# Performance work log

Hardware: AMD Instinct MI355X
Metric: run time of the kernel (lower is better)

## Reference

```python
import jax, jax.numpy as jnp
import numpy as np

T, TRACE, CTX = 4096, 64, 64


def setup_inputs() -> dict:
    key = jax.random.key(0)
    k0, k1, k2, k3 = jax.random.split(key, 4)
    state_re = jax.random.normal(k0, (T, TRACE, CTX), dtype=jnp.float32)
    state_im = jax.random.normal(k1, (T, TRACE, CTX), dtype=jnp.float32)
    x_re = jax.random.normal(k2, (T, TRACE, CTX), dtype=jnp.float32)
    x_im = jax.random.normal(k3, (T, TRACE, CTX), dtype=jnp.float32)
    # deterministic FFA param init (init_deterministic)
    a = jnp.linspace(1e-6, 0.5, TRACE).astype(jnp.float32)
    b = (2.0 * jnp.pi / jnp.linspace(1.0, 1000.0, CTX)).astype(jnp.float32)
    i = jnp.ones((T,), dtype=jnp.int32)          # carry step counter
    j = jnp.arange(T, dtype=jnp.int32)           # incoming time offsets
    return {"state_re": state_re, "state_im": state_im, "x_re": x_re,
            "x_im": x_im, "a": a, "b": b, "i": i, "j": j}


def reference(state_re, state_im, x_re, x_im, a, b, i, j):
    # gamma(t) = exp((-|a| + i*b) * t) expanded in real arithmetic
    t = j.astype(jnp.float32)[:, None, None]              # [T,1,1]
    decay = jnp.exp(-jnp.abs(a)[None, :, None] * t)       # [T,TRACE,1]
    theta = b[None, None, :] * t                          # [T,1,CTX]
    g_re = decay * jnp.cos(theta)                         # [T,TRACE,CTX]
    g_im = decay * jnp.sin(theta)
    # state * gamma + x  (complex multiply-add)
    new_re = state_re * g_re - state_im * g_im + x_re
    new_im = state_re * g_im + state_im * g_re + x_im
    # output: complex state stacked as (..., 2) = (re, im), plus updated counter
    return jnp.stack([new_re, new_im], axis=-1), j + i
```

## Files before the change

kernel.cpp:

```cpp
#include <hip/hip_runtime.h>
#include <math.h>

#define T_DIM 4096
#define TRACE 64
#define CTX   64
#define NELEM  (T_DIM * TRACE * CTX)
#define NGROUP (NELEM / 4)

typedef float f32x4 __attribute__((ext_vector_type(4)));

__global__ __launch_bounds__(256) void ffm_tables(
    const float* __restrict__ a, const float* __restrict__ b,
    const int*   __restrict__ iv, const int* __restrict__ jv,
    float* __restrict__ tcos, float* __restrict__ tsin,
    float* __restrict__ tdec, float* __restrict__ out_cnt)
{
    const int idx = blockIdx.x * 256 + threadIdx.x;
    const int t   = idx >> 6;
    const int k   = idx & 63;
    const float tf = (float)jv[t];
    float s, c;
    sincosf(b[k] * tf, &s, &c);
    tcos[idx] = c;
    tsin[idx] = s;
    tdec[idx] = expf(-fabsf(a[k]) * tf);
    if (k == 0) out_cnt[t] = (float)(jv[t] + iv[t]);
}

__global__ __launch_bounds__(256) void ffm_main(
    const float* __restrict__ sre_, const float* __restrict__ sim_,
    const float* __restrict__ xre_, const float* __restrict__ xim_,
    const float* __restrict__ tcos, const float* __restrict__ tsin,
    const float* __restrict__ tdec,
    float* __restrict__ out)
{
    const float4* __restrict__ sre = (const float4*)sre_;
    const float4* __restrict__ sim = (const float4*)sim_;
    const float4* __restrict__ xre = (const float4*)xre_;
    const float4* __restrict__ xim = (const float4*)xim_;
    f32x4* __restrict__ o = (f32x4*)out;

    const int stride = gridDim.x * 256;
    const int g0 = blockIdx.x * 256 + threadIdx.x;

    #pragma unroll 2
    for (int it = 0; it < NGROUP / (2048 * 256); ++it) {
        const int g  = g0 + it * stride;
        const int e  = g << 2;
        const int t  = e >> 12;
        const int tr = (e >> 6) & 63;
        const int c0 = e & 63;

        const float4 vc  = *(const float4*)(tcos + t * 64 + c0);
        const float4 vs  = *(const float4*)(tsin + t * 64 + c0);
        const float  dec = tdec[t * 64 + tr];

        const float4 vre = sre[g];
        const float4 vim = sim[g];
        const float4 vxr = xre[g];
        const float4 vxi = xim[g];

        const float gr0 = dec * vc.x, gi0 = dec * vs.x;
        const float gr1 = dec * vc.y, gi1 = dec * vs.y;
        const float gr2 = dec * vc.z, gi2 = dec * vs.z;
        const float gr3 = dec * vc.w, gi3 = dec * vs.w;

        f32x4 o0, o1;
        o0.x = fmaf(vre.x, gr0, fmaf(-vim.x, gi0, vxr.x));
        o0.y = fmaf(vre.x, gi0, fmaf( vim.x, gr0, vxi.x));
        o0.z = fmaf(vre.y, gr1, fmaf(-vim.y, gi1, vxr.y));
        o0.w = fmaf(vre.y, gi1, fmaf( vim.y, gr1, vxi.y));
        o1.x = fmaf(vre.z, gr2, fmaf(-vim.z, gi2, vxr.z));
        o1.y = fmaf(vre.z, gi2, fmaf( vim.z, gr2, vxi.z));
        o1.z = fmaf(vre.w, gr3, fmaf(-vim.w, gi3, vxr.w));
        o1.w = fmaf(vre.w, gi3, fmaf( vim.w, gr3, vxi.w));

        __builtin_nontemporal_store(o0, &o[2 * g + 0]);
        __builtin_nontemporal_store(o1, &o[2 * g + 1]);
    }
}

__global__ __launch_bounds__(256) void ffm_kernel_fallback(
    const float* __restrict__ state_re, const float* __restrict__ state_im,
    const float* __restrict__ x_re, const float* __restrict__ x_im,
    const float* __restrict__ a, const float* __restrict__ b,
    const int* __restrict__ ivec, const int* __restrict__ jvec,
    float* __restrict__ out, float* __restrict__ out_cnt)
{
    const int t   = blockIdx.x;
    const int tid = threadIdx.x;
    const float tf = (float)jvec[t];

    __shared__ float s_cos[CTX];
    __shared__ float s_sin[CTX];
    __shared__ float s_dec[TRACE];

    if (tid < CTX) {
        float theta = b[tid] * tf;
        float s, c;
        sincosf(theta, &s, &c);
        s_cos[tid] = c;
        s_sin[tid] = s;
    } else if (tid < CTX + TRACE) {
        int tr = tid - CTX;
        s_dec[tr] = expf(-fabsf(a[tr]) * tf);
    }
    if (tid == 0) out_cnt[t] = (float)(jvec[t] + ivec[t]);
    __syncthreads();

    const size_t base = (size_t)t * (TRACE * CTX);
    const float4* sre = (const float4*)(state_re + base);
    const float4* sim = (const float4*)(state_im + base);
    const float4* xre = (const float4*)(x_re + base);
    const float4* xim = (const float4*)(x_im + base);
    float4* o = (float4*)(out + base * 2);

    #pragma unroll
    for (int k = 0; k < 4; ++k) {
        const int g  = tid + k * 256;
        const int e  = g * 4;
        const int tr = e >> 6;
        const int c0 = e & 63;

        const float dec = s_dec[tr];
        const float4 vre = sre[g];
        const float4 vim = sim[g];
        const float4 vxr = xre[g];
        const float4 vxi = xim[g];

        const float gr0 = dec * s_cos[c0 + 0], gi0 = dec * s_sin[c0 + 0];
        const float gr1 = dec * s_cos[c0 + 1], gi1 = dec * s_sin[c0 + 1];
        const float gr2 = dec * s_cos[c0 + 2], gi2 = dec * s_sin[c0 + 2];
        const float gr3 = dec * s_cos[c0 + 3], gi3 = dec * s_sin[c0 + 3];

        float4 o0, o1;
        o0.x = fmaf(vre.x, gr0, fmaf(-vim.x, gi0, vxr.x));
        o0.y = fmaf(vre.x, gi0, fmaf( vim.x, gr0, vxi.x));
        o0.z = fmaf(vre.y, gr1, fmaf(-vim.y, gi1, vxr.y));
        o0.w = fmaf(vre.y, gi1, fmaf( vim.y, gr1, vxi.y));
        o1.x = fmaf(vre.z, gr2, fmaf(-vim.z, gi2, vxr.z));
        o1.y = fmaf(vre.z, gi2, fmaf( vim.z, gr2, vxi.z));
        o1.z = fmaf(vre.w, gr3, fmaf(-vim.w, gi3, vxr.w));
        o1.w = fmaf(vre.w, gi3, fmaf( vim.w, gr3, vxi.w));

        o[2 * g + 0] = o0;
        o[2 * g + 1] = o1;
    }
}

extern "C" void kernel_launch(void* const* d_in, const int* in_sizes, int n_in,
                              void* d_out, int out_size, void* d_ws, size_t ws_size,
                              hipStream_t stream) {
    const float* state_re = (const float*)d_in[0];
    const float* state_im = (const float*)d_in[1];
    const float* x_re     = (const float*)d_in[2];
    const float* x_im     = (const float*)d_in[3];
    const float* a        = (const float*)d_in[4];
    const float* b        = (const float*)d_in[5];
    const int*   iv       = (const int*)d_in[6];
    const int*   jv       = (const int*)d_in[7];

    float* out     = (float*)d_out;
    float* out_cnt = out + (size_t)T_DIM * TRACE * CTX * 2;

    const size_t tab_elems = (size_t)T_DIM * 64;
    const size_t need = 3 * tab_elems * sizeof(float);

    if (ws_size >= need) {
        float* tcos = (float*)d_ws;
        float* tsin = tcos + tab_elems;
        float* tdec = tsin + tab_elems;

        ffm_tables<<<T_DIM * 64 / 256, 256, 0, stream>>>(
            a, b, iv, jv, tcos, tsin, tdec, out_cnt);
        ffm_main<<<2048, 256, 0, stream>>>(
            state_re, state_im, x_re, x_im, tcos, tsin, tdec, out);
    } else {
        ffm_kernel_fallback<<<T_DIM, 256, 0, stream>>>(
            state_re, state_im, x_re, x_im, a, b, iv, jv, out, out_cnt);
    }
}
```

Baseline: 339.7 us.

## Map one block per time step in main kernel, drop nontemporal stores

Measured after the change: 329.7 us. -2.9%, faster.

```diff
diff --git a/kernel.cpp b/kernel.cpp
--- a/kernel.cpp
+++ b/kernel.cpp
@@ -4,10 +4,6 @@
 #define T_DIM 4096
 #define TRACE 64
 #define CTX   64
-#define NELEM  (T_DIM * TRACE * CTX)
-#define NGROUP (NELEM / 4)
-
-typedef float f32x4 __attribute__((ext_vector_type(4)));
 
 __global__ __launch_bounds__(256) void ffm_tables(
     const float* __restrict__ a, const float* __restrict__ b,
@@ -28,32 +24,36 @@
 }
 
 __global__ __launch_bounds__(256) void ffm_main(
-    const float* __restrict__ sre_, const float* __restrict__ sim_,
-    const float* __restrict__ xre_, const float* __restrict__ xim_,
+    const float* __restrict__ state_re, const float* __restrict__ state_im,
+    const float* __restrict__ x_re, const float* __restrict__ x_im,
     const float* __restrict__ tcos, const float* __restrict__ tsin,
     const float* __restrict__ tdec,
     float* __restrict__ out)
 {
-    const float4* __restrict__ sre = (const float4*)sre_;
-    const float4* __restrict__ sim = (const float4*)sim_;
-    const float4* __restrict__ xre = (const float4*)xre_;
-    const float4* __restrict__ xim = (const float4*)xim_;
-    f32x4* __restrict__ o = (f32x4*)out;
+    const int t   = blockIdx.x;
+    const int tid = threadIdx.x;
 
-    const int stride = gridDim.x * 256;
-    const int g0 = blockIdx.x * 256 + threadIdx.x;
+    const size_t base = (size_t)t * (TRACE * CTX);
+    const float4* sre = (const float4*)(state_re + base);
+    const float4* sim = (const float4*)(state_im + base);
+    const float4* xre = (const float4*)(x_re + base);
+    const float4* xim = (const float4*)(x_im + base);
+    float4* o = (float4*)(out + base * 2);
 
-    #pragma unroll 2
-    for (int it = 0; it < NGROUP / (2048 * 256); ++it) {
-        const int g  = g0 + it * stride;
-        const int e  = g << 2;
-        const int t  = e >> 12;
-        const int tr = (e >> 6) & 63;
-        const int c0 = e & 63;
+    const float4* tc = (const float4*)(tcos + t * 64);
+    const float4* ts = (const float4*)(tsin + t * 64);
+    const float*  td = tdec + t * 64;
 
-        const float4 vc  = *(const float4*)(tcos + t * 64 + c0);
-        const float4 vs  = *(const float4*)(tsin + t * 64 + c0);
-        const float  dec = tdec[t * 64 + tr];
+    #pragma unroll
+    for (int k = 0; k < 4; ++k) {
+        const int g  = tid + k * 256;
+        const int e  = g * 4;
+        const int tr = e >> 6;
+        const int c4 = (e & 63) >> 2;
+
+        const float  dec = td[tr];
+        const float4 vc  = tc[c4];
+        const float4 vs  = ts[c4];
 
         const float4 vre = sre[g];
         const float4 vim = sim[g];
@@ -65,7 +65,7 @@
         const float gr2 = dec * vc.z, gi2 = dec * vs.z;
         const float gr3 = dec * vc.w, gi3 = dec * vs.w;
 
-        f32x4 o0, o1;
+        float4 o0, o1;
         o0.x = fmaf(vre.x, gr0, fmaf(-vim.x, gi0, vxr.x));
         o0.y = fmaf(vre.x, gi0, fmaf( vim.x, gr0, vxi.x));
         o0.z = fmaf(vre.y, gr1, fmaf(-vim.y, gi1, vxr.y));
@@ -75,8 +75,8 @@
         o1.z = fmaf(vre.w, gr3, fmaf(-vim.w, gi3, vxr.w));
         o1.w = fmaf(vre.w, gi3, fmaf( vim.w, gr3, vxi.w));
 
-        __builtin_nontemporal_store(o0, &o[2 * g + 0]);
-        __builtin_nontemporal_store(o1, &o[2 * g + 1]);
+        o[2 * g + 0] = o0;
+        o[2 * g + 1] = o1;
     }
 }
 
@@ -173,7 +173,7 @@
 
         ffm_tables<<<T_DIM * 64 / 256, 256, 0, stream>>>(
             a, b, iv, jv, tcos, tsin, tdec, out_cnt);
-        ffm_main<<<2048, 256, 0, stream>>>(
+        ffm_main<<<T_DIM, 256, 0, stream>>>(
             state_re, state_im, x_re, x_im, tcos, tsin, tdec, out);
     } else {
         ffm_kernel_fallback<<<T_DIM, 256, 0, stream>>>(
```
